# Performance work log

Measured on AMD Instinct MI355X. Metric: run time of the kernel, lower is better.

The kernel has to match this reference:

```python
import jax, jax.numpy as jnp
import numpy as np

WINDOW_LEN = 256
HOP_LEN = 128
LOG_EPS = 1e-8


def setup_inputs() -> dict:
    key = jax.random.key(0)
    # (batch=64, eeg_channels=23, n_samples=30720)  ~ 2 min @ 256 Hz
    signal = jax.random.normal(key, (64, 23, 30720), dtype=jnp.float32)
    return {"signal": signal}


def _hanning(m):
    # matches np.hanning: symmetric Hann window of length m
    n = jnp.arange(m, dtype=jnp.float32)
    return 0.5 - 0.5 * jnp.cos(2.0 * jnp.pi * n / (m - 1))


def reference(signal):
    wl, hop = WINDOW_LEN, HOP_LEN
    window = _hanning(wl)
    n_windows = (signal.shape[-1] - wl) // hop + 1  # static
    # gather indices for all frames: (n_windows, wl)
    idx = jnp.arange(n_windows)[:, None] * hop + jnp.arange(wl)[None, :]
    frames = signal[..., idx] * window          # (..., n_windows, wl)
    spec = jnp.fft.rfft(frames, n=wl, axis=-1)  # (..., n_windows, wl//2+1) complex
    # log_scale=True branch of the module
    return jnp.log(jnp.abs(spec) + LOG_EPS) * 10.0
```

## Files before the change

### kernel.cpp

```cpp
#include <hip/hip_runtime.h>
#include <math.h>

#define WL     256
#define HOP    128
#define NW     239
#define NBINS  129
#define NSAMP  30720
#define NROWS  (64*23)

__global__ __launch_bounds__(64) void stft_kernel(const float* __restrict__ sig,
                                                  float* __restrict__ out) {
    const int l   = threadIdx.x;
    const int bid = blockIdx.x;
    const int row = bid / NW;
    const int w   = bid - row * NW;
    const float* __restrict__ src = sig + (size_t)row * NSAMP + (size_t)w * HOP;

    __shared__ __align__(8) float zre[128];
    __shared__ __align__(8) float zim[128];

    float2 xa = *reinterpret_cast<const float2*>(src + 2 * l);
    float2 xb = *reinterpret_cast<const float2*>(src + 2 * l + 128);
    float w0 = 0.5f - 0.5f * cospif((float)(4 * l)       * (1.0f / 255.0f));
    float w1 = 0.5f - 0.5f * cospif((float)(4 * l + 2)   * (1.0f / 255.0f));
    float w2 = 0.5f - 0.5f * cospif((float)(4 * l + 256) * (1.0f / 255.0f));
    float w3 = 0.5f - 0.5f * cospif((float)(4 * l + 258) * (1.0f / 255.0f));
    float v0r = xa.x * w0, v0i = xa.y * w1;
    float v1r = xb.x * w2, v1i = xb.y * w3;

    {
        float s, c;
        sincospif((float)l * (1.0f / 64.0f), &s, &c);
        float tr = v0r - v1r, ti = v0i - v1i;
        v0r += v1r; v0i += v1i;
        v1r = tr * c + ti * s;
        v1i = ti * c - tr * s;
    }

    #pragma unroll
    for (int m = 32; m >= 4; m >>= 1) {
        float s, c;
        sincospif((float)(l & (m - 1)) * (1.0f / (float)m), &s, &c);
        const bool up = (l & m) != 0;
        float p0r = __shfl_xor(v0r, m), p0i = __shfl_xor(v0i, m);
        float p1r = __shfl_xor(v1r, m), p1i = __shfl_xor(v1i, m);
        float dr = p0r - v0r, di = p0i - v0i;
        float wr = dr * c + di * s, wi = di * c - dr * s;
        v0r = up ? wr : (v0r + p0r);
        v0i = up ? wi : (v0i + p0i);
        dr = p1r - v1r; di = p1i - v1i;
        wr = dr * c + di * s; wi = di * c - dr * s;
        v1r = up ? wr : (v1r + p1r);
        v1i = up ? wi : (v1i + p1i);
    }

    {
        const bool up = (l & 2) != 0;
        const bool j1 = (l & 1) != 0;
        float p0r = __shfl_xor(v0r, 2), p0i = __shfl_xor(v0i, 2);
        float p1r = __shfl_xor(v1r, 2), p1i = __shfl_xor(v1i, 2);
        float dr = p0r - v0r, di = p0i - v0i;
        float wr = j1 ? di : dr, wi = j1 ? -dr : di;
        v0r = up ? wr : (v0r + p0r);
        v0i = up ? wi : (v0i + p0i);
        dr = p1r - v1r; di = p1i - v1i;
        wr = j1 ? di : dr; wi = j1 ? -dr : di;
        v1r = up ? wr : (v1r + p1r);
        v1i = up ? wi : (v1i + p1i);
    }

    {
        const bool up = (l & 1) != 0;
        float p0r = __shfl_xor(v0r, 1), p0i = __shfl_xor(v0i, 1);
        float p1r = __shfl_xor(v1r, 1), p1i = __shfl_xor(v1i, 1);
        v0r = up ? (p0r - v0r) : (v0r + p0r);
        v0i = up ? (p0i - v0i) : (v0i + p0i);
        v1r = up ? (p1r - v1r) : (v1r + p1r);
        v1i = up ? (p1i - v1i) : (v1i + p1i);
    }

    const int pn = (int)(__brev((unsigned)l) >> 26);
    reinterpret_cast<float2*>(zre)[pn] = make_float2(v0r, v1r);
    reinterpret_cast<float2*>(zim)[pn] = make_float2(v0i, v1i);
    __syncthreads();

    float* __restrict__ o = out + (size_t)bid * NBINS;
    #pragma unroll
    for (int q = 0; q < 2; ++q) {
        int k  = l + 64 * q;
        int km = (128 - k) & 127;
        float zkr = zre[k],  zki = zim[k];
        float zmr = zre[km], zmi = zim[km];
        float er  = 0.5f * (zkr + zmr);
        float ei  = 0.5f * (zki - zmi);
        float orr = 0.5f * (zki + zmi);
        float oi  = -0.5f * (zkr - zmr);
        float s, c;
        sincospif((float)k * (1.0f / 128.0f), &s, &c);
        float Xr = er + c * orr + s * oi;
        float Xi = ei + c * oi - s * orr;
        float mag = sqrtf(Xr * Xr + Xi * Xi);
        o[k] = __log2f(mag + 1e-8f) * 6.931471805599453f;
    }
    if (l == 0) {
        float Xr = zre[0] - zim[0];
        o[128] = __log2f(fabsf(Xr) + 1e-8f) * 6.931471805599453f;
    }
}

extern "C" void kernel_launch(void* const* d_in, const int* in_sizes, int n_in,
                              void* d_out, int out_size, void* d_ws, size_t ws_size,
                              hipStream_t stream) {
    const float* sig = (const float*)d_in[0];
    float* out = (float*)d_out;
    (void)in_sizes; (void)n_in; (void)out_size; (void)d_ws; (void)ws_size;
    const int nblocks = NROWS * NW;
    stft_kernel<<<dim3(nblocks), dim3(64), 0, stream>>>(sig, out);
}
```

Measured before the change: 463.2 us.

## Process multiple STFT frames per block and hoist window and twiddle computation

The launch changes from one 64-thread block per frame to a fixed grid of 8192 blocks, each looping over 43 consecutive frames. The Hann window weights, per-stage FFT twiddles and real-FFT post-processing twiddles are computed once per block instead of once per frame, which removes repeated sincospi/cospi work and per-block launch and scheduling overhead. The __syncthreads between the shared-memory writes and reads is dropped because each block is a single 64-lane wavefront. This relies on in-order LDS access within a wave. It also leaves fewer waves in flight to hide memory latency.

```diff
diff --git a/kernel.cpp b/kernel.cpp
--- a/kernel.cpp
+++ b/kernel.cpp
@@ -7,104 +7,129 @@
 #define NBINS  129
 #define NSAMP  30720
 #define NROWS  (64*23)
+#define NFRAMES (NROWS * NW)
+#define NBLOCKS 8192
+#define FPB     43
 
 __global__ __launch_bounds__(64) void stft_kernel(const float* __restrict__ sig,
                                                   float* __restrict__ out) {
-    const int l   = threadIdx.x;
-    const int bid = blockIdx.x;
-    const int row = bid / NW;
-    const int w   = bid - row * NW;
-    const float* __restrict__ src = sig + (size_t)row * NSAMP + (size_t)w * HOP;
+    const int l = threadIdx.x;
 
     __shared__ __align__(8) float zre[128];
     __shared__ __align__(8) float zim[128];
 
-    float2 xa = *reinterpret_cast<const float2*>(src + 2 * l);
-    float2 xb = *reinterpret_cast<const float2*>(src + 2 * l + 128);
-    float w0 = 0.5f - 0.5f * cospif((float)(4 * l)       * (1.0f / 255.0f));
-    float w1 = 0.5f - 0.5f * cospif((float)(4 * l + 2)   * (1.0f / 255.0f));
-    float w2 = 0.5f - 0.5f * cospif((float)(4 * l + 256) * (1.0f / 255.0f));
-    float w3 = 0.5f - 0.5f * cospif((float)(4 * l + 258) * (1.0f / 255.0f));
-    float v0r = xa.x * w0, v0i = xa.y * w1;
-    float v1r = xb.x * w2, v1i = xb.y * w3;
+    const float w0 = 0.5f - 0.5f * cospif((float)(4 * l)       * (1.0f / 255.0f));
+    const float w1 = 0.5f - 0.5f * cospif((float)(4 * l + 2)   * (1.0f / 255.0f));
+    const float w2 = 0.5f - 0.5f * cospif((float)(4 * l + 256) * (1.0f / 255.0f));
+    const float w3 = 0.5f - 0.5f * cospif((float)(4 * l + 258) * (1.0f / 255.0f));
+    float c64, s64;  sincospif((float)l * (1.0f / 64.0f), &s64, &c64);
+    float c32, s32;  sincospif((float)(l & 31) * (1.0f / 32.0f), &s32, &c32);
+    float c16, s16;  sincospif((float)(l & 15) * (1.0f / 16.0f), &s16, &c16);
+    float c8,  s8;   sincospif((float)(l & 7)  * (1.0f / 8.0f),  &s8,  &c8);
+    float c4,  s4;   sincospif((float)(l & 3)  * (1.0f / 4.0f),  &s4,  &c4);
+    float cu0, su0;  sincospif((float)l        * (1.0f / 128.0f), &su0, &cu0);
+    float cu1, su1;  sincospif((float)(l + 64) * (1.0f / 128.0f), &su1, &cu1);
+    const int pn  = (int)(__brev((unsigned)l) >> 26);
+    const int km0 = (128 - l) & 127;
+    const int km1 = 64 - l;
 
-    {
-        float s, c;
-        sincospif((float)l * (1.0f / 64.0f), &s, &c);
-        float tr = v0r - v1r, ti = v0i - v1i;
-        v0r += v1r; v0i += v1i;
-        v1r = tr * c + ti * s;
-        v1i = ti * c - tr * s;
-    }
+    const int f0   = blockIdx.x * FPB;
+    const int fend = (f0 + FPB < NFRAMES) ? f0 + FPB : NFRAMES;
 
-    #pragma unroll
-    for (int m = 32; m >= 4; m >>= 1) {
-        float s, c;
-        sincospif((float)(l & (m - 1)) * (1.0f / (float)m), &s, &c);
-        const bool up = (l & m) != 0;
-        float p0r = __shfl_xor(v0r, m), p0i = __shfl_xor(v0i, m);
-        float p1r = __shfl_xor(v1r, m), p1i = __shfl_xor(v1i, m);
-        float dr = p0r - v0r, di = p0i - v0i;
-        float wr = dr * c + di * s, wi = di * c - dr * s;
-        v0r = up ? wr : (v0r + p0r);
-        v0i = up ? wi : (v0i + p0i);
-        dr = p1r - v1r; di = p1i - v1i;
-        wr = dr * c + di * s; wi = di * c - dr * s;
-        v1r = up ? wr : (v1r + p1r);
-        v1i = up ? wi : (v1i + p1i);
-    }
+    for (int f = f0; f < fend; ++f) {
+        const int row = f / NW;
+        const int w   = f - row * NW;
+        const float* __restrict__ src = sig + (size_t)row * NSAMP + (size_t)w * HOP;
 
-    {
-        const bool up = (l & 2) != 0;
-        const bool j1 = (l & 1) != 0;
-        float p0r = __shfl_xor(v0r, 2), p0i = __shfl_xor(v0i, 2);
-        float p1r = __shfl_xor(v1r, 2), p1i = __shfl_xor(v1i, 2);
-        float dr = p0r - v0r, di = p0i - v0i;
-        float wr = j1 ? di : dr, wi = j1 ? -dr : di;
-        v0r = up ? wr : (v0r + p0r);
-        v0i = up ? wi : (v0i + p0i);
-        dr = p1r - v1r; di = p1i - v1i;
-        wr = j1 ? di : dr; wi = j1 ? -dr : di;
-        v1r = up ? wr : (v1r + p1r);
-        v1i = up ? wi : (v1i + p1i);
-    }
+        float2 xa = *reinterpret_cast<const float2*>(src + 2 * l);
+        float2 xb = *reinterpret_cast<const float2*>(src + 2 * l + 128);
+        float v0r = xa.x * w0, v0i = xa.y * w1;
+        float v1r = xb.x * w2, v1i = xb.y * w3;
 
-    {
-        const bool up = (l & 1) != 0;
-        float p0r = __shfl_xor(v0r, 1), p0i = __shfl_xor(v0i, 1);
-        float p1r = __shfl_xor(v1r, 1), p1i = __shfl_xor(v1i, 1);
-        v0r = up ? (p0r - v0r) : (v0r + p0r);
-        v0i = up ? (p0i - v0i) : (v0i + p0i);
-        v1r = up ? (p1r - v1r) : (v1r + p1r);
-        v1i = up ? (p1i - v1i) : (v1i + p1i);
-    }
+        {
+            float tr = v0r - v1r, ti = v0i - v1i;
+            v0r += v1r; v0i += v1i;
+            v1r = tr * c64 + ti * s64;
+            v1i = ti * c64 - tr * s64;
+        }
 
-    const int pn = (int)(__brev((unsigned)l) >> 26);
-    reinterpret_cast<float2*>(zre)[pn] = make_float2(v0r, v1r);
-    reinterpret_cast<float2*>(zim)[pn] = make_float2(v0i, v1i);
-    __syncthreads();
+        #define XSTAGE(m, cc, ss)                                         \
+        {                                                                 \
+            const bool up = (l & (m)) != 0;                               \
+            float p0r = __shfl_xor(v0r, (m)), p0i = __shfl_xor(v0i, (m)); \
+            float p1r = __shfl_xor(v1r, (m)), p1i = __shfl_xor(v1i, (m)); \
+            float dr = p0r - v0r, di = p0i - v0i;                         \
+            float wr = dr * (cc) + di * (ss), wi = di * (cc) - dr * (ss); \
+            v0r = up ? wr : (v0r + p0r);                                  \
+            v0i = up ? wi : (v0i + p0i);                                  \
+            dr = p1r - v1r; di = p1i - v1i;                               \
+            wr = dr * (cc) + di * (ss); wi = di * (cc) - dr * (ss);       \
+            v1r = up ? wr : (v1r + p1r);                                  \
+            v1i = up ? wi : (v1i + p1i);                                  \
+        }
+        XSTAGE(32, c32, s32)
+        XSTAGE(16, c16, s16)
+        XSTAGE(8,  c8,  s8)
+        XSTAGE(4,  c4,  s4)
+        #undef XSTAGE
 
-    float* __restrict__ o = out + (size_t)bid * NBINS;
-    #pragma unroll
-    for (int q = 0; q < 2; ++q) {
-        int k  = l + 64 * q;
-        int km = (128 - k) & 127;
-        float zkr = zre[k],  zki = zim[k];
-        float zmr = zre[km], zmi = zim[km];
-        float er  = 0.5f * (zkr + zmr);
-        float ei  = 0.5f * (zki - zmi);
-        float orr = 0.5f * (zki + zmi);
-        float oi  = -0.5f * (zkr - zmr);
-        float s, c;
-        sincospif((float)k * (1.0f / 128.0f), &s, &c);
-        float Xr = er + c * orr + s * oi;
-        float Xi = ei + c * oi - s * orr;
-        float mag = sqrtf(Xr * Xr + Xi * Xi);
-        o[k] = __log2f(mag + 1e-8f) * 6.931471805599453f;
-    }
-    if (l == 0) {
-        float Xr = zre[0] - zim[0];
-        o[128] = __log2f(fabsf(Xr) + 1e-8f) * 6.931471805599453f;
+        {
+            const bool up = (l & 2) != 0;
+            const bool j1 = (l & 1) != 0;
+            float p0r = __shfl_xor(v0r, 2), p0i = __shfl_xor(v0i, 2);
+            float p1r = __shfl_xor(v1r, 2), p1i = __shfl_xor(v1i, 2);
+            float dr = p0r - v0r, di = p0i - v0i;
+            float wr = j1 ? di : dr, wi = j1 ? -dr : di;
+            v0r = up ? wr : (v0r + p0r);
+            v0i = up ? wi : (v0i + p0i);
+            dr = p1r - v1r; di = p1i - v1i;
+            wr = j1 ? di : dr; wi = j1 ? -dr : di;
+            v1r = up ? wr : (v1r + p1r);
+            v1i = up ? wi : (v1i + p1i);
+        }
+
+        {
+            const bool up = (l & 1) != 0;
+            float p0r = __shfl_xor(v0r, 1), p0i = __shfl_xor(v0i, 1);
+            float p1r = __shfl_xor(v1r, 1), p1i = __shfl_xor(v1i, 1);
+            v0r = up ? (p0r - v0r) : (v0r + p0r);
+            v0i = up ? (p0i - v0i) : (v0i + p0i);
+            v1r = up ? (p1r - v1r) : (v1r + p1r);
+            v1i = up ? (p1i - v1i) : (v1i + p1i);
+        }
+
+        reinterpret_cast<float2*>(zre)[pn] = make_float2(v0r, v1r);
+        reinterpret_cast<float2*>(zim)[pn] = make_float2(v0i, v1i);
+
+        float* __restrict__ o = out + (size_t)f * NBINS;
+        {
+            float zkr = zre[l],   zki = zim[l];
+            float zmr = zre[km0], zmi = zim[km0];
+            float er  = 0.5f * (zkr + zmr);
+            float ei  = 0.5f * (zki - zmi);
+            float orr = 0.5f * (zki + zmi);
+            float oi  = -0.5f * (zkr - zmr);
+            float Xr = er + cu0 * orr + su0 * oi;
+            float Xi = ei + cu0 * oi - su0 * orr;
+            float mag = sqrtf(Xr * Xr + Xi * Xi);
+            o[l] = __log2f(mag + 1e-8f) * 6.931471805599453f;
+        }
+        {
+            float zkr = zre[l + 64], zki = zim[l + 64];
+            float zmr = zre[km1],    zmi = zim[km1];
+            float er  = 0.5f * (zkr + zmr);
+            float ei  = 0.5f * (zki - zmi);
+            float orr = 0.5f * (zki + zmi);
+            float oi  = -0.5f * (zkr - zmr);
+            float Xr = er + cu1 * orr + su1 * oi;
+            float Xi = ei + cu1 * oi - su1 * orr;
+            float mag = sqrtf(Xr * Xr + Xi * Xi);
+            o[l + 64] = __log2f(mag + 1e-8f) * 6.931471805599453f;
+        }
+        if (l == 0) {
+            float Xr = zre[0] - zim[0];
+            o[128] = __log2f(fabsf(Xr) + 1e-8f) * 6.931471805599453f;
+        }
     }
 }
 
@@ -114,6 +139,5 @@
     const float* sig = (const float*)d_in[0];
     float* out = (float*)d_out;
     (void)in_sizes; (void)n_in; (void)out_size; (void)d_ws; (void)ws_size;
-    const int nblocks = NROWS * NW;
-    stft_kernel<<<dim3(nblocks), dim3(64), 0, stream>>>(sig, out);
+    stft_kernel<<<dim3(NBLOCKS), dim3(64), 0, stream>>>(sig, out);
 }
```

Result: faster. 373.0 us (-19.5%).
